# Performance work log

Measured on AMD Instinct MI355X. Metric: run time of the kernel, lower is better.

The kernel has to match this reference:

```python
import jax, jax.numpy as jnp
import numpy as np

D_IN = 2048
D_OUT = 2048
NUM_HEADS = 16
HEAD_DIM = D_OUT // NUM_HEADS
CONTEXT_LENGTH = 4096
THETA_BASE = 10000.0


def _rope_tables(seq_len):
    half = HEAD_DIM // 2
    inv_freq = 1.0 / (THETA_BASE ** (jnp.arange(half, dtype=jnp.float32) / half))
    positions = jnp.arange(seq_len, dtype=jnp.float32)
    angles = positions[:, None] * inv_freq[None, :]          # [S, half]
    angles = jnp.concatenate([angles, angles], axis=-1)      # [S, HEAD_DIM]
    return jnp.cos(angles), jnp.sin(angles)


def _apply_rope(x, cos, sin):
    # x: [B, H, S, D]
    half = x.shape[-1] // 2
    x1, x2 = x[..., :half], x[..., half:]
    rotated = jnp.concatenate([-x2, x1], axis=-1)
    return x * cos[None, None, :, :] + rotated * sin[None, None, :, :]


def setup_inputs() -> dict:
    key = jax.random.key(0)
    ks = jax.random.split(key, 5)
    x = jax.random.normal(ks[0], (1, 4096, D_IN), dtype=jnp.float32)
    scale_in = 1.0 / np.sqrt(D_IN)
    scale_out = 1.0 / np.sqrt(D_OUT)
    w_q = jax.random.normal(ks[1], (D_OUT, D_IN), dtype=jnp.float32) * scale_in
    w_k = jax.random.normal(ks[2], (D_OUT, D_IN), dtype=jnp.float32) * scale_in
    w_v = jax.random.normal(ks[3], (D_OUT, D_IN), dtype=jnp.float32) * scale_in
    w_o = jax.random.normal(ks[4], (D_IN, D_OUT), dtype=jnp.float32) * scale_out
    return {"x": x, "w_q": w_q, "w_k": w_k, "w_v": w_v, "w_o": w_o}


def reference(x, w_q, w_k, w_v, w_o):
    b, s, _ = x.shape
    cos, sin = _rope_tables(s)

    def split_heads(t):  # [B,S,D_OUT] -> [B,H,S,HEAD_DIM]
        return t.reshape(b, s, NUM_HEADS, HEAD_DIM).transpose(0, 2, 1, 3)

    q = split_heads(jnp.einsum('bsd,od->bso', x, w_q))
    k = split_heads(jnp.einsum('bsd,od->bso', x, w_k))
    v = split_heads(jnp.einsum('bsd,od->bso', x, w_v))

    q = _apply_rope(q, cos, sin)
    k = _apply_rope(k, cos, sin)

    scores = jnp.einsum('bhqd,bhkd->bhqk', q, k) / jnp.sqrt(jnp.float32(HEAD_DIM))
    causal = jnp.tril(jnp.ones((s, s), dtype=bool))
    scores = jnp.where(causal[None, None, :, :], scores, -jnp.inf)
    attn = jax.nn.softmax(scores, axis=-1)

    ctx = jnp.einsum('bhqk,bhkd->bhqd', attn, v)  # [B,H,S,HEAD_DIM]
    ctx = ctx.transpose(0, 2, 1, 3).reshape(b, s, D_OUT)
    return jnp.einsum('bso,do->bsd', ctx, w_o)
```

## Files before the change

### kernel.cpp

```cpp
#include <hip/hip_runtime.h>
#include <hip/hip_bf16.h>
#include <stdint.h>

#define SEQ 4096
#define DM 2048
#define NH 16
#define HD 128

typedef __attribute__((ext_vector_type(4)))  float f32x4;
typedef __attribute__((ext_vector_type(16))) float f32x16;
typedef __attribute__((ext_vector_type(8)))  short bf16x8;
typedef __attribute__((ext_vector_type(4)))  float float4_t;
typedef __attribute__((ext_vector_type(4)))  short s16x4;
typedef __attribute__((ext_vector_type(2)))  int   i32x2;
typedef __attribute__((ext_vector_type(2)))  unsigned u32x2;

__device__ __forceinline__ short f2bf(float f) {
  union { float f; unsigned u; } c; c.f = f;
  unsigned u = c.u;
  u += 0x7FFFu + ((u >> 16) & 1u);
  return (short)(u >> 16);
}

__device__ __forceinline__ int cvtpk(float lo, float hi) {
  int r;
  asm("v_cvt_pk_bf16_f32 %0, %1, %2" : "=v"(r) : "v"(lo), "v"(hi));
  return r;
}

__device__ __forceinline__ float exp2r(float x) {
  return __builtin_amdgcn_exp2f(x);
}

__device__ __forceinline__ void async16(const void* g, void* l) {
  __builtin_amdgcn_global_load_lds((const __attribute__((address_space(1))) void*)g,
                                   (__attribute__((address_space(3))) void*)l, 16, 0, 0);
}

__global__ __launch_bounds__(256) void rope_tables_kernel(float2* __restrict__ tab) {
  int idx = blockIdx.x * 256 + threadIdx.x;
  int s = idx >> 6, j = idx & 63;
  float invf = expf(-(float)j * (9.210340371976184f / 64.0f));
  float ang = (float)s * invf;
  tab[idx] = make_float2(cosf(ang), sinf(ang));
}

__global__ __launch_bounds__(256) void f32_to_bf16_kernel(const float* __restrict__ in,
                                                          short* __restrict__ out, int n4) {
  int stride = gridDim.x * 256;
  for (int i = blockIdx.x * 256 + threadIdx.x; i < n4; i += stride) {
    float4_t v = ((const float4_t*)in)[i];
    s16x4 r;
    #pragma unroll
    for (int u = 0; u < 4; u++) r[u] = f2bf(v[u]);
    ((s16x4*)out)[i] = r;
  }
}

__global__ __launch_bounds__(256) void w3_to_bf16_kernel(
    const float* __restrict__ wq, const float* __restrict__ wk,
    const float* __restrict__ wv, short* __restrict__ out) {
  const int n4w = DM * DM / 4;
  int stride = gridDim.x * 256;
  for (int i = blockIdx.x * 256 + threadIdx.x; i < 3 * n4w; i += stride) {
    int j = i >> 20;
    int loc = i & (n4w - 1);
    const float* src = (j == 0) ? wq : (j == 1) ? wk : wv;
    float4_t v = ((const float4_t*)src)[loc];
    s16x4 r;
    #pragma unroll
    for (int u = 0; u < 4; u++) r[u] = f2bf(v[u]);
    ((s16x4*)out)[i] = r;
  }
}

__global__ __launch_bounds__(512) void gemm_qkv_kernel(
    const short* __restrict__ A, const short* __restrict__ B,
    short* __restrict__ Qout, short* __restrict__ Kout, short* __restrict__ VTout,
    const float2* __restrict__ tab, int region) {
  constexpr int NN = DM, K = DM, MM = SEQ;
  __shared__ __align__(16) char LB[147456];
  const int t = threadIdx.x, lane = t & 63, w = t >> 6;
  const int wm = w >> 1, wn = w & 1;
  const size_t Mbase = (size_t)blockIdx.x * 256;
  const int ry  = (region < 0) ? (blockIdx.y >> 4) : region;
  const int nyl = (region < 0) ? (blockIdx.y & 15) : blockIdx.y;
  const size_t Bbase = (size_t)blockIdx.y * 128;
  const size_t Nbase = (size_t)nyl * 128;
  const int nt = K / 64;

  auto stageA = [&](int kt, int half) {
    const int buf = kt % 3, k0 = kt * 64;
    #pragma unroll
    for (int it = 0; it < 2; it++) {
      const int ob = half * 16384 + it * 8192 + w * 1024;
      const int o = ob + lane * 16;
      const int row = o >> 7;
      const int col = (o & 127) ^ ((row & 7) << 4);
      async16((const char*)A + ((Mbase + row) * (size_t)K + k0) * 2 + col,
              LB + buf * 32768 + ob);
    }
  };
  auto stageB = [&](int kt) {
    const int buf = kt % 3, k0 = kt * 64;
    #pragma unroll
    for (int it = 0; it < 2; it++) {
      const int ob = it * 8192 + w * 1024;
      const int o = ob + lane * 16;
      const int row = o >> 7;
      const int col = (o & 127) ^ ((row & 7) << 4);
      async16((const char*)B + ((Bbase + row) * (size_t)K + k0) * 2 + col,
              LB + 98304 + buf * 16384 + ob);
    }
  };

  f32x4 acc[4][4] = {};

  stageA(0, 0); stageA(0, 1); stageB(0);
  stageA(1, 0); stageA(1, 1); stageB(1);
  asm volatile("s_waitcnt vmcnt(6)" ::: "memory");
  __builtin_amdgcn_s_barrier();

  for (int kt = 0; kt < nt; kt++) {
    const char* AsB = LB + (kt % 3) * 32768;
    const char* BsB = LB + 98304 + (kt % 3) * 16384;
    const bool pre = (kt + 2 < nt);
    bf16x8 a[2][4], b[2][2], b2[2][2];

    #pragma unroll
    for (int ks = 0; ks < 2; ks++)
      #pragma unroll
      for (int m = 0; m < 4; m++) {
        int row = wm * 64 + m * 16 + (lane & 15);
        a[ks][m] = *(const bf16x8*)(AsB + row * 128
                    + ((ks * 64 + (lane >> 4) * 16) ^ ((row & 7) << 4)));
      }
    #pragma unroll
    for (int ks = 0; ks < 2; ks++)
      #pragma unroll
      for (int n = 0; n < 2; n++) {
        int row = n * 32 + wn * 16 + (lane & 15);
        b[ks][n] = *(const bf16x8*)(BsB + row * 128
                    + ((ks * 64 + (lane >> 4) * 16) ^ ((row & 7) << 4)));
      }
    if (pre) { stageA(kt + 2, 0); stageA(kt + 2, 1); stageB(kt + 2); }

    __builtin_amdgcn_s_setprio(1);
    #pragma unroll
    for (int ks = 0; ks < 2; ks++)
      #pragma unroll
      for (int m = 0; m < 4; m++)
        #pragma unroll
        for (int n = 0; n < 2; n++)
          acc[m][n] = __builtin_amdgcn_mfma_f32_16x16x32_bf16(
              a[ks][m], b[ks][n], acc[m][n], 0, 0, 0);
    __builtin_amdgcn_s_setprio(0);

    #pragma unroll
    for (int ks = 0; ks < 2; ks++)
      #pragma unroll
      for (int n = 0; n < 2; n++) {
        int row = (n + 2) * 32 + wn * 16 + (lane & 15);
        b2[ks][n] = *(const bf16x8*)(BsB + row * 128
                     + ((ks * 64 + (lane >> 4) * 16) ^ ((row & 7) << 4)));
      }
    __builtin_amdgcn_s_setprio(1);
    #pragma unroll
    for (int ks = 0; ks < 2; ks++)
      #pragma unroll
      for (int m = 0; m < 4; m++)
        #pragma unroll
        for (int n = 0; n < 2; n++)
          acc[m][n + 2] = __builtin_amdgcn_mfma_f32_16x16x32_bf16(
              a[ks][m], b2[ks][n], acc[m][n + 2], 0, 0, 0);
    __builtin_amdgcn_s_setprio(0);

    if (kt + 1 < nt) {
      if (pre) asm volatile("s_waitcnt vmcnt(6) lgkmcnt(0)" ::: "memory");
      else     asm volatile("s_waitcnt vmcnt(0) lgkmcnt(0)" ::: "memory");
      __builtin_amdgcn_sched_barrier(0);
      __builtin_amdgcn_s_barrier();
    }
  }

  if (ry < 2) {
    const float SC = (ry == 0) ? 0.12751746f : 1.0f;
    short* C = (ry == 0) ? Qout : Kout;
    #pragma unroll
    for (int m = 0; m < 4; m++)
      #pragma unroll
      for (int n = 0; n < 2; n++)
        #pragma unroll
        for (int j = 0; j < 4; j++) {
          int row = (int)Mbase + wm * 64 + m * 16 + (lane >> 4) * 4 + j;
          int dj = n * 32 + wn * 16 + (lane & 15);
          float2 cs = tab[row * 64 + dj];
          float cc = cs.x * SC, ss = cs.y * SC;
          float r1 = acc[m][n][j], r2 = acc[m][n + 2][j];
          C[(size_t)row * NN + Nbase + dj]      = f2bf(r1 * cc - r2 * ss);
          C[(size_t)row * NN + Nbase + dj + 64] = f2bf(r2 * cc + r1 * ss);
        }
  } else {
    #pragma unroll
    for (int m = 0; m < 4; m++)
      #pragma unroll
      for (int n = 0; n < 4; n++)
        #pragma unroll
        for (int j = 0; j < 4; j++) {
          size_t row = Mbase + wm * 64 + m * 16 + (lane >> 4) * 4 + j;
          size_t col = Nbase + n * 32 + wn * 16 + (lane & 15);
          VTout[col * (size_t)MM + row] = f2bf(acc[m][n][j]);
        }
  }
}

__global__ __launch_bounds__(512) void gemm_out_kernel(
    const short* __restrict__ A, const short* __restrict__ B,
    float* __restrict__ Cp) {
  constexpr int NN = DM, K = DM;
  __shared__ __align__(16) char LB[147456];
  const int t = threadIdx.x, lane = t & 63, w = t >> 6;
  const int wm = w >> 1, wn = w & 1;
  const size_t Mbase = (size_t)blockIdx.x * 256;
  const size_t Nbase = (size_t)blockIdx.y * 128;
  const int nt = K / 64;

  auto stageA = [&](int kt, int half) {
    const int buf = kt % 3, k0 = kt * 64;
    #pragma unroll
    for (int it = 0; it < 2; it++) {
      const int ob = half * 16384 + it * 8192 + w * 1024;
      const int o = ob + lane * 16;
      const int row = o >> 7;
      const int col = (o & 127) ^ ((row & 7) << 4);
      async16((const char*)A + ((Mbase + row) * (size_t)K + k0) * 2 + col,
              LB + buf * 32768 + ob);
    }
  };
  auto stageB = [&](int kt) {
    const int buf = kt % 3, k0 = kt * 64;
    #pragma unroll
    for (int it = 0; it < 2; it++) {
      const int ob = it * 8192 + w * 1024;
      const int o = ob + lane * 16;
      const int row = o >> 7;
      const int col = (o & 127) ^ ((row & 7) << 4);
      async16((const char*)B + ((Nbase + row) * (size_t)K + k0) * 2 + col,
              LB + 98304 + buf * 16384 + ob);
    }
  };

  f32x4 acc[4][4] = {};

  stageA(0, 0); stageA(0, 1); stageB(0);
  stageA(1, 0); stageA(1, 1); stageB(1);
  asm volatile("s_waitcnt vmcnt(6)" ::: "memory");
  __builtin_amdgcn_s_barrier();

  for (int kt = 0; kt < nt; kt++) {
    const char* AsB = LB + (kt % 3) * 32768;
    const char* BsB = LB + 98304 + (kt % 3) * 16384;
    const bool pre = (kt + 2 < nt);
    bf16x8 a[2][4], b[2][2], b2[2][2];

    #pragma unroll
    for (int ks = 0; ks < 2; ks++)
      #pragma unroll
      for (int m = 0; m < 4; m++) {
        int row = wm * 64 + m * 16 + (lane & 15);
        a[ks][m] = *(const bf16x8*)(AsB + row * 128
                    + ((ks * 64 + (lane >> 4) * 16) ^ ((row & 7) << 4)));
      }
    #pragma unroll
    for (int ks = 0; ks < 2; ks++)
      #pragma unroll
      for (int n = 0; n < 2; n++) {
        int row = n * 32 + wn * 16 + (lane & 15);
        b[ks][n] = *(const bf16x8*)(BsB + row * 128
                    + ((ks * 64 + (lane >> 4) * 16) ^ ((row & 7) << 4)));
      }
    if (pre) { stageA(kt + 2, 0); stageA(kt + 2, 1); stageB(kt + 2); }

    __builtin_amdgcn_s_setprio(1);
    #pragma unroll
    for (int ks = 0; ks < 2; ks++)
      #pragma unroll
      for (int m = 0; m < 4; m++)
        #pragma unroll
        for (int n = 0; n < 2; n++)
          acc[m][n] = __builtin_amdgcn_mfma_f32_16x16x32_bf16(
              a[ks][m], b[ks][n], acc[m][n], 0, 0, 0);
    __builtin_amdgcn_s_setprio(0);

    #pragma unroll
    for (int ks = 0; ks < 2; ks++)
      #pragma unroll
      for (int n = 0; n < 2; n++) {
        int row = (n + 2) * 32 + wn * 16 + (lane & 15);
        b2[ks][n] = *(const bf16x8*)(BsB + row * 128
                     + ((ks * 64 + (lane >> 4) * 16) ^ ((row & 7) << 4)));
      }
    __builtin_amdgcn_s_setprio(1);
    #pragma unroll
    for (int ks = 0; ks < 2; ks++)
      #pragma unroll
      for (int m = 0; m < 4; m++)
        #pragma unroll
        for (int n = 0; n < 2; n++)
          acc[m][n + 2] = __builtin_amdgcn_mfma_f32_16x16x32_bf16(
              a[ks][m], b2[ks][n], acc[m][n + 2], 0, 0, 0);
    __builtin_amdgcn_s_setprio(0);

    if (kt + 1 < nt) {
      if (pre) asm volatile("s_waitcnt vmcnt(6) lgkmcnt(0)" ::: "memory");
      else     asm volatile("s_waitcnt vmcnt(0) lgkmcnt(0)" ::: "memory");
      __builtin_amdgcn_sched_barrier(0);
      __builtin_amdgcn_s_barrier();
    }
  }

  #pragma unroll
  for (int m = 0; m < 4; m++)
    #pragma unroll
    for (int n = 0; n < 4; n++)
      #pragma unroll
      for (int j = 0; j < 4; j++) {
        size_t row = Mbase + wm * 64 + m * 16 + (lane >> 4) * 4 + j;
        size_t col = Nbase + n * 32 + wn * 16 + (lane & 15);
        Cp[row * NN + col] = acc[m][n][j];
      }
}

__global__ __launch_bounds__(512) void flash_attn9_kernel(
    const short* __restrict__ Q, const short* __restrict__ K,
    const short* __restrict__ VT, short* __restrict__ O) {
  __shared__ __align__(16) char LB[65536];
  const int t = threadIdx.x, lane = t & 63, w = t >> 6;
  const int hi = lane >> 5, c31 = lane & 31;
  const int s = w & 3, v = w >> 2;
  const int id = blockIdx.x;
  const int h  = (id & 7) * 2 + ((id >> 3) & 1);
  const int pr = (id >> 4) & 15;
  const int qt = (id < 256) ? pr : (31 - pr);

  auto stage = [&](int kt, int buf) {
    #pragma unroll
    for (int it = 0; it < 2; it++) {
      const int ob = it * 8192 + w * 1024;
      const int o  = ob + lane * 16;
      const int row = o >> 8;
      const int xs = (o & 255) ^ ((row & 15) << 4);
      { const size_t src = ((size_t)(kt * 64 + row) * DM + h * HD) * 2 + xs;
        async16((const char*)K + src, LB + buf * 16384 + ob); }
      { const int d = 2 * row + (xs >> 7);
        const size_t src = ((size_t)(h * HD + d) * SEQ + (size_t)kt * 64) * 2
                         + (size_t)(xs & 127);
        async16((const char*)VT + src, LB + 32768 + buf * 16384 + ob); }
    }
  };

  const int q0 = qt * 128;
  const int nt = 2 * (qt + 1);
  const int qrow = q0 + s * 32 + c31;

  stage(0, 0);

  bf16x8 qf[8];
  #pragma unroll
  for (int ss = 0; ss < 8; ss++)
    qf[ss] = *(const bf16x8*)(Q + (size_t)qrow * DM + h * HD + ss * 16 + hi * 8);

  f32x16 oacc[4] = {};
  float m = -3.0e38f, l = 0.f;

  __syncthreads();

  for (int kt = 0; kt < nt; kt++) {
    const int buf = kt & 1;
    if (kt + 1 < nt) stage(kt + 1, buf ^ 1);

    if (kt * 64 + v * 32 <= q0 + s * 32 + 31) {
      const char* KsB = LB + buf * 16384;
      const char* VsB = LB + 32768 + buf * 16384;

      f32x16 sacc = {};
      __builtin_amdgcn_s_setprio(1);
      #pragma unroll
      for (int ss = 0; ss < 8; ss++) {
        int row = v * 32 + c31;
        bf16x8 kf = *(const bf16x8*)(KsB + row * 256
                                     + ((ss * 32 + hi * 16) ^ ((row & 15) << 4)));
        sacc = __builtin_amdgcn_mfma_f32_32x32x16_bf16(kf, qf[ss], sacc, 0, 0, 0);
      }
      __builtin_amdgcn_s_setprio(0);

      float t0[8];
      #pragma unroll
      for (int r = 0; r < 8; r++) t0[r] = fmaxf(sacc[r], sacc[r + 8]);
      #pragma unroll
      for (int d = 4; d > 0; d >>= 1)
        #pragma unroll
        for (int r = 0; r < 4; r++) if (r < d) t0[r] = fmaxf(t0[r], t0[r + d]);
      float mx = t0[0];
      i32x2 mm = __builtin_amdgcn_permlane32_swap(__float_as_int(mx), __float_as_int(mx),
                                                  false, false);
      mx = fmaxf(__int_as_float(mm.x), __int_as_float(mm.y));

      if (__any(mx > m + 11.5416f)) {
        float mn = fmaxf(m, mx);
        float al = exp2r(m - mn);
        m = mn; l *= al;
        #pragma unroll
        for (int g = 0; g < 4; g++)
          #pragma unroll
          for (int r = 0; r < 16; r++) oacc[g][r] *= al;
      }

      const int rel = qrow - kt * 64 - v * 32;
      const bool maskT = (kt * 64 + v * 32 + 31) > (q0 + s * 32);
      #pragma unroll
      for (int r = 0; r < 16; r++) {
        float e = exp2r(sacc[r] - m);
        if (maskT) {
          int kl = (r & 3) + 8 * (r >> 2) + 4 * hi;
          e = (kl > rel) ? 0.f : e;
        }
        sacc[r] = e;
      }

      float s0[8];
      #pragma unroll
      for (int r = 0; r < 8; r++) s0[r] = sacc[r] + sacc[r + 8];
      #pragma unroll
      for (int d = 4; d > 0; d >>= 1)
        #pragma unroll
        for (int r = 0; r < 4; r++) if (r < d) s0[r] = s0[r] + s0[r + d];
      l += s0[0];

      bf16x8 pa[2];
      #pragma unroll
      for (int sg = 0; sg < 2; sg++) {
        int q0a = cvtpk(sacc[8 * sg + 0], sacc[8 * sg + 1]);
        int q1a = cvtpk(sacc[8 * sg + 2], sacc[8 * sg + 3]);
        int q0b = cvtpk(sacc[8 * sg + 4], sacc[8 * sg + 5]);
        int q1b = cvtpk(sacc[8 * sg + 6], sacc[8 * sg + 7]);
        i32x2 r0 = __builtin_amdgcn_permlane32_swap(q0a, q0b, false, false);
        i32x2 r1 = __builtin_amdgcn_permlane32_swap(q1a, q1b, false, false);
        union { int d[4]; bf16x8 vv; } u;
        u.d[0] = r0.x; u.d[1] = r1.x; u.d[2] = r0.y; u.d[3] = r1.y;
        pa[sg] = u.vv;
      }

      __builtin_amdgcn_s_setprio(1);
      #pragma unroll
      for (int ks = 0; ks < 2; ks++)
        #pragma unroll
        for (int g = 0; g < 4; g++) {
          int d = g * 32 + c31;
          int row = d >> 1;
          int x = (d & 1) * 128 + v * 64 + ks * 32 + hi * 16;
          bf16x8 vf = *(const bf16x8*)(VsB + row * 256 + (x ^ ((row & 15) << 4)));
          oacc[g] = __builtin_amdgcn_mfma_f32_32x32x16_bf16(vf, pa[ks], oacc[g], 0, 0, 0);
        }
      __builtin_amdgcn_s_setprio(0);
    }
    __syncthreads();
  }

  i32x2 lr = __builtin_amdgcn_permlane32_swap(__float_as_int(l), __float_as_int(l),
                                              false, false);
  l = __int_as_float(lr.x) + __int_as_float(lr.y);

  #pragma unroll
  for (int round = 0; round < 2; round++) {
    const int reg = s & 1;
    const bool active = (s >> 1) == round;
    if (active && v == 1) {
      float* Op = (float*)(LB + reg * 16384);
      #pragma unroll
      for (int g = 0; g < 4; g++)
        #pragma unroll
        for (int rr = 0; rr < 16; rr++) {
          int d = g * 32 + (rr & 3) + 8 * (rr >> 2) + 4 * hi;
          Op[d * 32 + c31] = oacc[g][rr];
        }
      if (hi == 0) {
        float* mm2 = (float*)(LB + 32768 + reg * 256) + c31 * 2;
        mm2[0] = m; mm2[1] = l;
      }
    }
    __syncthreads();
    if (active && v == 0) {
      const float* mm2 = (const float*)(LB + 32768 + reg * 256) + c31 * 2;
      float lB = mm2[1];
      float mB = (lB > 0.f) ? mm2[0] : -3.0e38f;
      float ms = fmaxf(m, mB);
      float aA = exp2r(m - ms), aB = exp2r(mB - ms);
      float linv = 1.0f / (l * aA + lB * aB);
      float sA = aA * linv, sB = aB * linv;
      const float* Op = (const float*)(LB + reg * 16384);
      #pragma unroll
      for (int g = 0; g < 4; g++)
        #pragma unroll
        for (int tt = 0; tt < 4; tt++) {
          float o[4];
          #pragma unroll
          for (int e = 0; e < 4; e++) {
            int d = g * 32 + e + 8 * tt + 4 * hi;
            o[e] = oacc[g][4 * tt + e] * sA + Op[d * 32 + c31] * sB;
          }
          u32x2 pk;
          pk.x = (unsigned)cvtpk(o[0], o[1]);
          pk.y = (unsigned)cvtpk(o[2], o[3]);
          *(u32x2*)(O + (size_t)qrow * DM + h * HD + g * 32 + tt * 8 + hi * 4) = pk;
        }
    }
    __syncthreads();
  }
}

extern "C" void kernel_launch(void* const* d_in, const int* in_sizes, int n_in,
                              void* d_out, int out_size, void* d_ws, size_t ws_size,
                              hipStream_t stream) {
  const float* x  = (const float*)d_in[0];
  const float* wq = (const float*)d_in[1];
  const float* wk = (const float*)d_in[2];
  const float* wv = (const float*)d_in[3];
  const float* wo = (const float*)d_in[4];
  float* out = (float*)d_out;

  const size_t SQDMs = (size_t)SEQ * DM;
  short* Qb   = (short*)d_ws;
  short* Kb   = Qb + SQDMs;
  short* VTb  = Kb + SQDMs;
  short* Cb   = VTb + SQDMs;
  short* xbf  = Cb + SQDMs;
  short* wbuf = xbf + SQDMs;

  const bool fused = ws_size >= (size_t)107 * 1024 * 1024;
  float2* tab = (float2*)(wbuf + (fused ? (size_t)3 * DM * DM : (size_t)DM * DM));

  rope_tables_kernel<<<SEQ * 64 / 256, 256, 0, stream>>>(tab);
  f32_to_bf16_kernel<<<2048, 256, 0, stream>>>(x, xbf, (int)(SQDMs / 4));

  if (fused) {
    w3_to_bf16_kernel<<<2048, 256, 0, stream>>>(wq, wk, wv, wbuf);
    gemm_qkv_kernel<<<dim3(SEQ / 256, 48), 512, 0, stream>>>(
        xbf, wbuf, Qb, Kb, VTb, tab, -1);
  } else {
    f32_to_bf16_kernel<<<2048, 256, 0, stream>>>(wq, wbuf, DM * DM / 4);
    gemm_qkv_kernel<<<dim3(SEQ / 256, 16), 512, 0, stream>>>(
        xbf, wbuf, Qb, Kb, VTb, tab, 0);
    f32_to_bf16_kernel<<<2048, 256, 0, stream>>>(wk, wbuf, DM * DM / 4);
    gemm_qkv_kernel<<<dim3(SEQ / 256, 16), 512, 0, stream>>>(
        xbf, wbuf, Qb, Kb, VTb, tab, 1);
    f32_to_bf16_kernel<<<2048, 256, 0, stream>>>(wv, wbuf, DM * DM / 4);
    gemm_qkv_kernel<<<dim3(SEQ / 256, 16), 512, 0, stream>>>(
        xbf, wbuf, Qb, Kb, VTb, tab, 2);
  }

  flash_attn9_kernel<<<512, 512, 0, stream>>>(Qb, Kb, VTb, Cb);

  f32_to_bf16_kernel<<<2048, 256, 0, stream>>>(wo, wbuf, DM * DM / 4);
  gemm_out_kernel<<<dim3(SEQ / 256, DM / 128), 512, 0, stream>>>(Cb, wbuf, out);
}
```

Measured before the change: 271.9 us.

## Replace fused QKV GEMM with 256x192-tile 12-wave kernel plus separate RoPE pass

The fused QKV projection now uses a new 768-thread kernel with 256x192 output tiles, K-step 32 and triple-buffered LDS. The launch grid becomes 16x32 blocks instead of 16x48. RoPE rotation and the Q scaling are taken out of the GEMM epilogue and moved into a separate elementwise kernel that reads and rewrites Q and K in bf16. This is meant to improve GEMM tiling and occupancy, at the cost of an extra pass over Q and K in memory and an extra bf16 rounding before the rotation. The epilogue also uses scalar 2-byte stores, including strided stores for V transposed, which may be slow.

```diff
diff --git a/kernel.cpp b/kernel.cpp
--- a/kernel.cpp
+++ b/kernel.cpp
@@ -20,6 +20,11 @@
   unsigned u = c.u;
   u += 0x7FFFu + ((u >> 16) & 1u);
   return (short)(u >> 16);
+}
+__device__ __forceinline__ float bf2f(short s) {
+  union { unsigned u; float f; } c;
+  c.u = ((unsigned)(unsigned short)s) << 16;
+  return c.f;
 }
 
 __device__ __forceinline__ int cvtpk(float lo, float hi) {
@@ -74,6 +79,137 @@
   }
 }
 
+__global__ __launch_bounds__(256) void rope_apply_kernel(
+    short* __restrict__ Q, short* __restrict__ K, const float2* __restrict__ tab) {
+  int idx = blockIdx.x * 256 + threadIdx.x;
+  int j4 = (idx & 15) * 4;
+  int h  = (idx >> 4) & 15;
+  int s  = idx >> 8;
+  const float SCQ = 0.12751746f;
+  size_t base = (size_t)s * DM + h * HD;
+  s16x4 q1 = *(s16x4*)(Q + base + j4),      q2 = *(s16x4*)(Q + base + 64 + j4);
+  s16x4 k1 = *(s16x4*)(K + base + j4),      k2 = *(s16x4*)(K + base + 64 + j4);
+  s16x4 o1, o2, p1, p2;
+  #pragma unroll
+  for (int u = 0; u < 4; u++) {
+    float2 cs = tab[s * 64 + j4 + u];
+    float c = cs.x, sn = cs.y;
+    float a = bf2f(q1[u]), b = bf2f(q2[u]);
+    o1[u] = f2bf((a * c - b * sn) * SCQ);
+    o2[u] = f2bf((b * c + a * sn) * SCQ);
+    a = bf2f(k1[u]); b = bf2f(k2[u]);
+    p1[u] = f2bf(a * c - b * sn);
+    p2[u] = f2bf(b * c + a * sn);
+  }
+  *(s16x4*)(Q + base + j4) = o1;  *(s16x4*)(Q + base + 64 + j4) = o2;
+  *(s16x4*)(K + base + j4) = p1;  *(s16x4*)(K + base + 64 + j4) = p2;
+}
+
+__global__ __launch_bounds__(768) void gemm_qkv12_kernel(
+    const short* __restrict__ A, const short* __restrict__ B,
+    short* __restrict__ Qout, short* __restrict__ Kout, short* __restrict__ VTout) {
+  constexpr int K = DM, MM = SEQ;
+  __shared__ __align__(16) char LB[86016];
+  const int t = threadIdx.x, lane = t & 63, w = t >> 6;
+  const int wm = w & 3, wn = w >> 2;
+  const size_t Mbase = (size_t)blockIdx.x * 256;
+  const size_t Bbase = (size_t)blockIdx.y * 192;
+  const int nt = K / 32;
+
+  auto stage = [&](int kt) {
+    const int buf = kt % 3, k0 = kt * 32;
+    if (w < 8) {
+      #pragma unroll
+      for (int it = 0; it < 2; it++) {
+        const int ob = w * 2048 + it * 1024;
+        const int o = ob + lane * 16;
+        const int lr = o >> 7;
+        const int xs = (o & 127) ^ ((lr & 7) << 4);
+        const int r = 2 * lr + (xs >> 6);
+        async16((const char*)A + ((Mbase + r) * (size_t)K + k0) * 2 + (xs & 63),
+                LB + buf * 28672 + ob);
+      }
+    } else {
+      #pragma unroll
+      for (int it = 0; it < 3; it++) {
+        const int ob = (w - 8) * 3072 + it * 1024;
+        const int o = ob + lane * 16;
+        const int lr = o >> 7;
+        const int xs = (o & 127) ^ ((lr & 7) << 4);
+        const int r = 2 * lr + (xs >> 6);
+        async16((const char*)B + ((Bbase + r) * (size_t)K + k0) * 2 + (xs & 63),
+                LB + buf * 28672 + 16384 + ob);
+      }
+    }
+  };
+
+  f32x4 acc[4][4] = {};
+
+  stage(0); stage(1);
+  if (w < 8) asm volatile("s_waitcnt vmcnt(2)" ::: "memory");
+  else       asm volatile("s_waitcnt vmcnt(3)" ::: "memory");
+  __builtin_amdgcn_s_barrier();
+
+  for (int kt = 0; kt < nt; kt++) {
+    const char* bufA = LB + (kt % 3) * 28672;
+    const char* bufB = bufA + 16384;
+    const bool pre = (kt + 2 < nt);
+    bf16x8 a[4], b[4];
+
+    const int cb = (lane >> 4) * 16;
+    #pragma unroll
+    for (int m = 0; m < 4; m++) {
+      int r = wm * 64 + m * 16 + (lane & 15);
+      a[m] = *(const bf16x8*)(bufA + (r >> 1) * 128
+               + ((((r & 1) * 64) + cb) ^ (((r >> 1) & 7) << 4)));
+    }
+    #pragma unroll
+    for (int n = 0; n < 4; n++) {
+      int r = wn * 64 + n * 16 + (lane & 15);
+      b[n] = *(const bf16x8*)(bufB + (r >> 1) * 128
+               + ((((r & 1) * 64) + cb) ^ (((r >> 1) & 7) << 4)));
+    }
+    if (pre) stage(kt + 2);
+
+    __builtin_amdgcn_s_setprio(1);
+    #pragma unroll
+    for (int m = 0; m < 4; m++)
+      #pragma unroll
+      for (int n = 0; n < 4; n++)
+        acc[m][n] = __builtin_amdgcn_mfma_f32_16x16x32_bf16(
+            a[m], b[n], acc[m][n], 0, 0, 0);
+    __builtin_amdgcn_s_setprio(0);
+
+    if (kt + 1 < nt) {
+      if (pre) {
+        if (w < 8) asm volatile("s_waitcnt vmcnt(2) lgkmcnt(0)" ::: "memory");
+        else       asm volatile("s_waitcnt vmcnt(3) lgkmcnt(0)" ::: "memory");
+      } else {
+        asm volatile("s_waitcnt vmcnt(0) lgkmcnt(0)" ::: "memory");
+      }
+      __builtin_amdgcn_sched_barrier(0);
+      __builtin_amdgcn_s_barrier();
+    }
+  }
+
+  #pragma unroll
+  for (int m = 0; m < 4; m++)
+    #pragma unroll
+    for (int n = 0; n < 4; n++) {
+      const int brow0 = (int)Bbase + wn * 64 + n * 16;
+      const int reg = brow0 >> 11;
+      #pragma unroll
+      for (int j = 0; j < 4; j++) {
+        size_t srow = Mbase + wm * 64 + m * 16 + (lane >> 4) * 4 + j;
+        int col = (brow0 + (lane & 15)) & 2047;
+        short v = f2bf(acc[m][n][j]);
+        if (reg == 0)      Qout[srow * DM + col] = v;
+        else if (reg == 1) Kout[srow * DM + col] = v;
+        else               VTout[(size_t)col * MM + srow] = v;
+      }
+    }
+}
+
 __global__ __launch_bounds__(512) void gemm_qkv_kernel(
     const short* __restrict__ A, const short* __restrict__ B,
     short* __restrict__ Qout, short* __restrict__ Kout, short* __restrict__ VTout,
@@ -83,10 +219,9 @@
   const int t = threadIdx.x, lane = t & 63, w = t >> 6;
   const int wm = w >> 1, wn = w & 1;
   const size_t Mbase = (size_t)blockIdx.x * 256;
-  const int ry  = (region < 0) ? (blockIdx.y >> 4) : region;
-  const int nyl = (region < 0) ? (blockIdx.y & 15) : blockIdx.y;
+  const int ry  = region;
   const size_t Bbase = (size_t)blockIdx.y * 128;
-  const size_t Nbase = (size_t)nyl * 128;
+  const size_t Nbase = (size_t)blockIdx.y * 128;
   const int nt = K / 64;
 
   auto stageA = [&](int kt, int half) {
@@ -545,8 +680,9 @@
 
   if (fused) {
     w3_to_bf16_kernel<<<2048, 256, 0, stream>>>(wq, wk, wv, wbuf);
-    gemm_qkv_kernel<<<dim3(SEQ / 256, 48), 512, 0, stream>>>(
-        xbf, wbuf, Qb, Kb, VTb, tab, -1);
+    gemm_qkv12_kernel<<<dim3(SEQ / 256, 32), 768, 0, stream>>>(
+        xbf, wbuf, Qb, Kb, VTb);
+    rope_apply_kernel<<<SEQ * NH * 16 / 256, 256, 0, stream>>>(Qb, Kb, tab);
   } else {
     f32_to_bf16_kernel<<<2048, 256, 0, stream>>>(wq, wbuf, DM * DM / 4);
     gemm_qkv_kernel<<<dim3(SEQ / 256, 16), 512, 0, stream>>>(
```

Result: slower. 291.1 us (+7.0%).
